# Kernel optimization log

Measured on AMD Instinct MI355X. Metric: run time of the kernel, lower is better.

The kernel has to match this reference:

```python
import jax, jax.numpy as jnp
import numpy as np

B, T, N, K, H, C = 32, 8, 1024, 20, 64, 14
EPS = 1e-5


def _bn(h, g, b):
    # eval-mode BatchNorm1d with running_mean=0, running_var=1
    return h * (g / jnp.sqrt(1.0 + EPS)) + b


def setup_inputs() -> dict:
    key = jax.random.key(0)
    ks = jax.random.split(key, 8)
    x = jax.random.normal(ks[0], (B, T, N, 3), jnp.float32)
    batch = jnp.repeat(jnp.arange(B, dtype=jnp.int64), 2 * N)
    s = 0.05
    W1 = jax.random.normal(ks[1], (6, H), jnp.float32) * s
    b1 = jnp.zeros((H,), jnp.float32)
    g1 = jnp.ones((H,), jnp.float32)
    be1 = jnp.zeros((H,), jnp.float32)
    Wa = jax.random.normal(ks[2], ((T - 1) * H, 512), jnp.float32) * s
    ba = jnp.zeros((512,), jnp.float32)
    ga = jnp.ones((512,), jnp.float32)
    bea = jnp.zeros((512,), jnp.float32)
    Wb = jax.random.normal(ks[3], (512, 256), jnp.float32) * s
    bb = jnp.zeros((256,), jnp.float32)
    gb = jnp.ones((256,), jnp.float32)
    beb = jnp.zeros((256,), jnp.float32)
    Wc = jax.random.normal(ks[4], (256, C), jnp.float32) * s
    bc = jnp.zeros((C,), jnp.float32)
    return dict(x=x, batch=batch, W1=W1, b1=b1, g1=g1, be1=be1,
                Wa=Wa, ba=ba, ga=ga, bea=bea, Wb=Wb, bb=bb, gb=gb, beb=beb,
                Wc=Wc, bc=bc)


def _timestep(xyz1, xyz2, W1, b1, g1, be1):
    # xyz1, xyz2: [B, N, 3]. kNN of each xyz1 point among xyz2 points.
    d2 = (jnp.sum(xyz1 * xyz1, -1)[:, :, None]
          + jnp.sum(xyz2 * xyz2, -1)[:, None, :]
          - 2.0 * jnp.einsum('bnd,bmd->bnm', xyz1, xyz2))  # [B,N,N]
    _, idx = jax.lax.top_k(-d2, K)                          # [B,N,K]
    neigh = jax.vmap(lambda pts, ii: pts[ii])(xyz2, idx)    # [B,N,K,3]
    # PyG EdgeConv with edge (source=row in xyz1, target=col in xyz2):
    # message = MLP(cat(x_i, x_j - x_i)) with x_i = neighbor (xyz2), x_j = center (xyz1)
    feat = jnp.concatenate([neigh, xyz1[:, :, None, :] - neigh], axis=-1)  # [B,N,K,6]
    h = _bn(jax.nn.relu(feat @ W1 + b1), g1, be1)            # [B,N,K,H]
    # max-aggr per target node then global_max_pool per graph == max over all edges;
    # isolated nodes contribute the zero fill of scatter-max -> clamp at 0.
    return jnp.maximum(jnp.max(h, axis=(1, 2)), 0.0)         # [B,H]


def reference(x, batch, W1, b1, g1, be1, Wa, ba, ga, bea, Wb, bb, gb, beb, Wc, bc):
    outs = []
    for i in range(1, T):
        outs.append(_timestep(x[:, i], x[:, i - 1], W1, b1, g1, be1))
    s_t = jnp.concatenate(outs, axis=1)                      # [B,(T-1)*H]
    h = _bn(jax.nn.relu(s_t @ Wa + ba), ga, bea)             # Dropout = identity (eval)
    h = _bn(jax.nn.relu(h @ Wb + bb), gb, beb)
    logits = h @ Wc + bc
    return jax.nn.log_softmax(logits, axis=1)
```

## Files before the change

### kernel.cpp

```cpp
#include <hip/hip_runtime.h>

#define BB 32
#define TT 8
#define NN 1024
#define KNN 20
#define HH 64
#define CLS 14

__device__ __constant__ float kEPS = 1e-5f;

__device__ __forceinline__ unsigned flipbits(unsigned u) {
    return u ^ ((unsigned)((int)u >> 31) | 0x80000000u);
}
__device__ __forceinline__ float unflip(unsigned fu) {
    const unsigned u = (fu & 0x80000000u) ? (fu ^ 0x80000000u) : ~fu;
    return __uint_as_float(u);
}
__device__ __forceinline__ int mbcnt64(unsigned long long m) {
    return (int)__builtin_amdgcn_mbcnt_hi((unsigned)(m >> 32),
            __builtin_amdgcn_mbcnt_lo((unsigned)m, 0u));
}

__device__ __forceinline__ void fallback20(unsigned fd[16], int lane, unsigned* nb) {
    for (int kk = 0; kk < KNN; ++kk) {
        unsigned bv = fd[0];
        int bi = 0;
        #pragma unroll
        for (int i = 1; i < 16; ++i)
            if (fd[i] < bv) { bv = fd[i]; bi = i; }
        unsigned bj = (unsigned)(bi * 64 + lane);
        #pragma unroll
        for (int off = 32; off >= 1; off >>= 1) {
            const unsigned ov = __shfl_xor(bv, off, 64);
            const unsigned oj = __shfl_xor(bj, off, 64);
            if (ov < bv || (ov == bv && oj < bj)) { bv = ov; bj = oj; }
        }
        if (lane == 0) nb[kk] = bj;
        #pragma unroll
        for (int i = 0; i < 16; ++i)
            if (bj == (unsigned)(i * 64 + lane)) fd[i] = 0xFFFFFFFFu;
    }
}

__global__ __launch_bounds__(256, 4) void knn_edge_kernel(
    const float* __restrict__ x,
    const float* __restrict__ W1,
    const float* __restrict__ b1,
    const float* __restrict__ g1,
    const float* __restrict__ be1,
    float* __restrict__ acc)
{
    __shared__ float4 pts[NN];
    __shared__ unsigned long long keybuf[4][64];
    __shared__ unsigned nbuf[4][KNN];
    __shared__ unsigned smax[HH];

    const int chunk = blockIdx.x;
    const int b     = blockIdx.y;
    const int t     = blockIdx.z;

    const int tid  = threadIdx.x;
    const int lane = tid & 63;
    const int wave = tid >> 6;

    for (int i = tid; i < NN; i += 256) {
        const float* p = x + (((size_t)b * TT + t) * NN + i) * 3;
        const float px = p[0], py = p[1], pz = p[2];
        pts[i] = make_float4(px, py, pz, px * px + py * py + pz * pz);
    }
    if (tid < HH) smax[tid] = 0u;
    __syncthreads();

    const float w3 = W1[3 * HH + lane], w4 = W1[4 * HH + lane],
                w5 = W1[5 * HH + lane];
    const float b1l   = b1[lane];
    const float scale = g1[lane] / sqrtf(1.0f + kEPS);
    const float be1l  = be1[lane];
    const float sgn = (scale >= 0.0f) ? 1.0f : -1.0f;
    const float w03 = sgn * (W1[0 * HH + lane] - w3),
                w14 = sgn * (W1[1 * HH + lane] - w4),
                w25 = sgn * (W1[2 * HH + lane] - w5);

    float zmax = -3.0e38f;

    const int n0 = chunk * 64 + wave * 16;
    for (int p = 0; p < 16; ++p) {
        const int n = n0 + p;
        const float* c = x + (((size_t)b * TT + (t + 1)) * NN + n) * 3;
        const float cx = c[0], cy = c[1], cz = c[2];
        const float s1 = cx * cx + cy * cy + cz * cz;
        const float n2x = -2.0f * cx, n2y = -2.0f * cy, n2z = -2.0f * cz;

        float d[16];
        float mnf = 3.0e38f;
        #pragma unroll
        for (int i = 0; i < 16; ++i) {
            const float4 q = pts[i * 64 + lane];
            d[i] = fmaf(n2x, q.x, fmaf(n2y, q.y, fmaf(n2z, q.z, s1 + q.w)));
            mnf = fminf(mnf, d[i]);
        }
        const unsigned mn = flipbits(__float_as_uint(mnf));

        unsigned pp = 0;
        int krem = 19;
        #pragma unroll
        for (int bit = 31; bit >= 20; --bit) {
            const unsigned long long z = __ballot(((mn ^ pp) >> bit) == 0u);
            const int c0 = (int)__popcll(z);
            if (krem >= c0) { pp |= (1u << bit); krem -= c0; }
        }
        const float ubf = unflip(pp | 0xFFFFFu);

        int base = 0;
        #pragma unroll
        for (int i = 0; i < 16; ++i) {
            const bool pr = d[i] <= ubf;
            const unsigned long long mk = __ballot(pr);
            if (pr) {
                const int pos = base + mbcnt64(mk);
                if (pos < 64) keybuf[wave][pos] =
                    ((unsigned long long)flipbits(__float_as_uint(d[i])) << 32)
                    | (unsigned)(i * 64 + lane);
            }
            base += (int)__popcll(mk);
        }

        if (base <= 64) {
            const unsigned long long mykey = keybuf[wave][lane];
            int rank = 0;
            for (int j = 0; j < base; ++j) {
                const unsigned long long kj = keybuf[wave][j];
                rank += (kj < mykey) ? 1 : 0;
            }
            if (lane < base && rank < KNN)
                nbuf[wave][rank] = (unsigned)mykey & 1023u;
        } else {
            unsigned fd[16];
            #pragma unroll
            for (int i = 0; i < 16; ++i) fd[i] = flipbits(__float_as_uint(d[i]));
            fallback20(fd, lane, &nbuf[wave][0]);
        }

        const float mb = sgn * fmaf(cx, w3, fmaf(cy, w4, fmaf(cz, w5, b1l)));
        #pragma unroll
        for (int kk = 0; kk < KNN; ++kk) {
            const int j = (int)nbuf[wave][kk];
            const float4 q = pts[j];
            const float z = fmaf(q.x, w03, fmaf(q.y, w14, fmaf(q.z, w25, mb)));
            zmax = fmaxf(zmax, z);
        }
    }

    const float r  = fmaxf(sgn * zmax, 0.0f);
    const float h  = fmaf(r, scale, be1l);
    const float cm = fmaxf(h, 0.0f);
    atomicMax(&smax[lane], __float_as_uint(cm));
    __syncthreads();
    if (tid < HH) {
        unsigned* dst = (unsigned*)(acc + ((size_t)b * 448 + t * 64 + tid));
        atomicMax(dst, smax[tid]);
    }
}

__global__ __launch_bounds__(512) void head_kernel(
    const float* __restrict__ acc,
    const float* __restrict__ Wa, const float* __restrict__ ba,
    const float* __restrict__ ga, const float* __restrict__ bea,
    const float* __restrict__ Wb, const float* __restrict__ bb,
    const float* __restrict__ gb, const float* __restrict__ beb,
    const float* __restrict__ Wc, const float* __restrict__ bc,
    float* __restrict__ out)
{
    __shared__ float s0[448];
    __shared__ float h1[512];
    __shared__ float h2[256];
    __shared__ float lg[CLS];
    __shared__ float red[2];

    const int b   = blockIdx.x;
    const int tid = threadIdx.x;
    const float inv = 1.0f / sqrtf(1.0f + kEPS);

    if (tid < 448) s0[tid] = acc[(size_t)b * 448 + tid];
    __syncthreads();

    {
        float s = ba[tid];
        for (int d = 0; d < 448; ++d) s = fmaf(s0[d], Wa[d * 512 + tid], s);
        s = fmaxf(s, 0.0f);
        h1[tid] = fmaf(s, ga[tid] * inv, bea[tid]);
    }
    __syncthreads();
    if (tid < 256) {
        float s = bb[tid];
        for (int d = 0; d < 512; ++d) s = fmaf(h1[d], Wb[d * 256 + tid], s);
        s = fmaxf(s, 0.0f);
        h2[tid] = fmaf(s, gb[tid] * inv, beb[tid]);
    }
    __syncthreads();
    if (tid < CLS) {
        float s = bc[tid];
        for (int d = 0; d < 256; ++d) s = fmaf(h2[d], Wc[d * CLS + tid], s);
        lg[tid] = s;
    }
    __syncthreads();
    if (tid == 0) {
        float m = lg[0];
        for (int j = 1; j < CLS; ++j) m = fmaxf(m, lg[j]);
        float ssum = 0.0f;
        for (int j = 0; j < CLS; ++j) ssum += expf(lg[j] - m);
        red[0] = m;
        red[1] = logf(ssum);
    }
    __syncthreads();
    if (tid < CLS) out[(size_t)b * CLS + tid] = lg[tid] - red[0] - red[1];
}

extern "C" void kernel_launch(void* const* d_in, const int* in_sizes, int n_in,
                              void* d_out, int out_size, void* d_ws, size_t ws_size,
                              hipStream_t stream) {
    const float* x   = (const float*)d_in[0];
    const float* W1  = (const float*)d_in[2];
    const float* b1  = (const float*)d_in[3];
    const float* g1  = (const float*)d_in[4];
    const float* be1 = (const float*)d_in[5];
    const float* Wa  = (const float*)d_in[6];
    const float* ba  = (const float*)d_in[7];
    const float* ga  = (const float*)d_in[8];
    const float* bea = (const float*)d_in[9];
    const float* Wb  = (const float*)d_in[10];
    const float* bb  = (const float*)d_in[11];
    const float* gb  = (const float*)d_in[12];
    const float* beb = (const float*)d_in[13];
    const float* Wc  = (const float*)d_in[14];
    const float* bc  = (const float*)d_in[15];
    float* out = (float*)d_out;
    float* acc = (float*)d_ws;

    hipMemsetAsync(acc, 0, (size_t)BB * 448 * sizeof(float), stream);

    dim3 grid(16, BB, 7);
    knn_edge_kernel<<<grid, 256, 0, stream>>>(x, W1, b1, g1, be1, acc);
    head_kernel<<<BB, 512, 0, stream>>>(acc, Wa, ba, ga, bea,
                                        Wb, bb, gb, beb, Wc, bc, out);
}
```

Baseline: 233.9 us.

## Process four query points per wave pass, recomputing distances instead of holding them

```diff
diff --git a/kernel.cpp b/kernel.cpp
--- a/kernel.cpp
+++ b/kernel.cpp
@@ -51,7 +51,7 @@
     float* __restrict__ acc)
 {
     __shared__ float4 pts[NN];
-    __shared__ unsigned long long keybuf[4][64];
+    __shared__ unsigned long long keybuf[4][4][64];
     __shared__ unsigned nbuf[4][KNN];
     __shared__ unsigned smax[HH];
 
@@ -84,70 +84,104 @@
     float zmax = -3.0e38f;
 
     const int n0 = chunk * 64 + wave * 16;
-    for (int p = 0; p < 16; ++p) {
-        const int n = n0 + p;
-        const float* c = x + (((size_t)b * TT + (t + 1)) * NN + n) * 3;
-        const float cx = c[0], cy = c[1], cz = c[2];
-        const float s1 = cx * cx + cy * cy + cz * cz;
-        const float n2x = -2.0f * cx, n2y = -2.0f * cy, n2z = -2.0f * cz;
-
-        float d[16];
-        float mnf = 3.0e38f;
+    for (int g = 0; g < 4; ++g) {
+        const float* c = x + (((size_t)b * TT + (t + 1)) * NN + (n0 + 4 * g)) * 3;
+        float cx[4], cy[4], cz[4], s1[4];
+        #pragma unroll
+        for (int p = 0; p < 4; ++p) {
+            cx[p] = c[3 * p + 0];
+            cy[p] = c[3 * p + 1];
+            cz[p] = c[3 * p + 2];
+            s1[p] = cx[p] * cx[p] + cy[p] * cy[p] + cz[p] * cz[p];
+        }
+
+        float mins[4] = {3.0e38f, 3.0e38f, 3.0e38f, 3.0e38f};
         #pragma unroll
         for (int i = 0; i < 16; ++i) {
             const float4 q = pts[i * 64 + lane];
-            d[i] = fmaf(n2x, q.x, fmaf(n2y, q.y, fmaf(n2z, q.z, s1 + q.w)));
-            mnf = fminf(mnf, d[i]);
-        }
-        const unsigned mn = flipbits(__float_as_uint(mnf));
-
-        unsigned pp = 0;
-        int krem = 19;
+            #pragma unroll
+            for (int p = 0; p < 4; ++p) {
+                const float d = fmaf(-2.0f * cx[p], q.x,
+                                fmaf(-2.0f * cy[p], q.y,
+                                fmaf(-2.0f * cz[p], q.z, s1[p] + q.w)));
+                mins[p] = fminf(mins[p], d);
+            }
+        }
+        asm volatile("" ::: "memory");
+
+        unsigned mnf[4];
+        #pragma unroll
+        for (int p = 0; p < 4; ++p) mnf[p] = flipbits(__float_as_uint(mins[p]));
+        unsigned ppx[4] = {0u, 0u, 0u, 0u};
+        int krem[4] = {19, 19, 19, 19};
         #pragma unroll
         for (int bit = 31; bit >= 20; --bit) {
-            const unsigned long long z = __ballot(((mn ^ pp) >> bit) == 0u);
-            const int c0 = (int)__popcll(z);
-            if (krem >= c0) { pp |= (1u << bit); krem -= c0; }
-        }
-        const float ubf = unflip(pp | 0xFFFFFu);
-
-        int base = 0;
+            #pragma unroll
+            for (int p = 0; p < 4; ++p) {
+                const unsigned long long z = __ballot(((mnf[p] ^ ppx[p]) >> bit) == 0u);
+                const int c0 = (int)__popcll(z);
+                if (krem[p] >= c0) { ppx[p] |= (1u << bit); krem[p] -= c0; }
+            }
+        }
+        float ubf[4];
+        #pragma unroll
+        for (int p = 0; p < 4; ++p) ubf[p] = unflip(ppx[p] | 0xFFFFFu);
+
+        int base[4] = {0, 0, 0, 0};
         #pragma unroll
         for (int i = 0; i < 16; ++i) {
-            const bool pr = d[i] <= ubf;
-            const unsigned long long mk = __ballot(pr);
-            if (pr) {
-                const int pos = base + mbcnt64(mk);
-                if (pos < 64) keybuf[wave][pos] =
-                    ((unsigned long long)flipbits(__float_as_uint(d[i])) << 32)
-                    | (unsigned)(i * 64 + lane);
-            }
-            base += (int)__popcll(mk);
-        }
-
-        if (base <= 64) {
-            const unsigned long long mykey = keybuf[wave][lane];
-            int rank = 0;
-            for (int j = 0; j < base; ++j) {
-                const unsigned long long kj = keybuf[wave][j];
-                rank += (kj < mykey) ? 1 : 0;
-            }
-            if (lane < base && rank < KNN)
-                nbuf[wave][rank] = (unsigned)mykey & 1023u;
-        } else {
-            unsigned fd[16];
-            #pragma unroll
-            for (int i = 0; i < 16; ++i) fd[i] = flipbits(__float_as_uint(d[i]));
-            fallback20(fd, lane, &nbuf[wave][0]);
-        }
-
-        const float mb = sgn * fmaf(cx, w3, fmaf(cy, w4, fmaf(cz, w5, b1l)));
-        #pragma unroll
-        for (int kk = 0; kk < KNN; ++kk) {
-            const int j = (int)nbuf[wave][kk];
-            const float4 q = pts[j];
-            const float z = fmaf(q.x, w03, fmaf(q.y, w14, fmaf(q.z, w25, mb)));
-            zmax = fmaxf(zmax, z);
+            const float4 q = pts[i * 64 + lane];
+            #pragma unroll
+            for (int p = 0; p < 4; ++p) {
+                const float d = fmaf(-2.0f * cx[p], q.x,
+                                fmaf(-2.0f * cy[p], q.y,
+                                fmaf(-2.0f * cz[p], q.z, s1[p] + q.w)));
+                const bool pr = d <= ubf[p];
+                const unsigned long long mk = __ballot(pr);
+                if (pr) {
+                    const int pos = base[p] + mbcnt64(mk);
+                    if (pos < 64) keybuf[wave][p][pos] =
+                        ((unsigned long long)flipbits(__float_as_uint(d)) << 32)
+                        | (unsigned)(i * 64 + lane);
+                }
+                base[p] += (int)__popcll(mk);
+            }
+        }
+        asm volatile("" ::: "memory");
+
+        #pragma unroll
+        for (int p = 0; p < 4; ++p) {
+            if (base[p] <= 64) {
+                const unsigned long long mykey = keybuf[wave][p][lane];
+                int rank = 0;
+                for (int j = 0; j < base[p]; ++j) {
+                    const unsigned long long kj = keybuf[wave][p][j];
+                    rank += (kj < mykey) ? 1 : 0;
+                }
+                if (lane < base[p] && rank < KNN)
+                    nbuf[wave][rank] = (unsigned)mykey & 1023u;
+            } else {
+                unsigned fd[16];
+                #pragma unroll
+                for (int i = 0; i < 16; ++i) {
+                    const float4 q = pts[i * 64 + lane];
+                    const float d = fmaf(-2.0f * cx[p], q.x,
+                                    fmaf(-2.0f * cy[p], q.y,
+                                    fmaf(-2.0f * cz[p], q.z, s1[p] + q.w)));
+                    fd[i] = flipbits(__float_as_uint(d));
+                }
+                fallback20(fd, lane, &nbuf[wave][0]);
+            }
+
+            const float mb = sgn * fmaf(cx[p], w3, fmaf(cy[p], w4,
+                                        fmaf(cz[p], w5, b1l)));
+            #pragma unroll
+            for (int kk = 0; kk < KNN; ++kk) {
+                const int j = (int)nbuf[wave][kk];
+                const float4 q = pts[j];
+                const float z = fmaf(q.x, w03, fmaf(q.y, w14, fmaf(q.z, w25, mb)));
+                zmax = fmaxf(zmax, z);
+            }
         }
     }
 
```

New measurement: 825.9 us. 253% more time.
